# Kernel optimization log

Hardware: AMD Instinct MI355X
Metric: run time of the kernel (lower is better)

The kernel has to match this reference:

```python
import jax, jax.numpy as jnp
import numpy as np

EPS = 1e-5

@jax.custom_vjp
def binarize(x):
    # sign quantization: {-1, +1} (0 -> +1), as in BinaryNet Binarize
    return jnp.where(x >= 0, 1.0, -1.0).astype(x.dtype)

def _bin_fwd(x):
    return binarize(x), x

def _bin_bwd(res, g):
    # straight-through estimator with hardtanh clipping
    return (g * (jnp.abs(res) <= 1.0).astype(g.dtype),)

binarize.defvjp(_bin_fwd, _bin_bwd)


def batchnorm(x, gamma, beta):
    # BatchNorm1d, training mode: biased batch statistics over the batch axis
    mu = jnp.mean(x, axis=0)
    var = jnp.var(x, axis=0)
    return (x - mu) * jax.lax.rsqrt(var + EPS) * gamma + beta


def setup_inputs() -> dict:
    key = jax.random.key(0)
    ks = jax.random.split(key, 5)
    B, IND, HID, OUT = 16384, 768, 4096, 10
    return {
        "x": jax.random.normal(ks[0], (B, 784), jnp.float32),
        "w1": jax.random.normal(ks[1], (HID, IND), jnp.float32) * 0.05,
        "w2": jax.random.normal(ks[2], (HID, HID), jnp.float32) * 0.05,
        "w3": jax.random.normal(ks[3], (HID, HID), jnp.float32) * 0.05,
        "w4": jax.random.normal(ks[4], (OUT, HID), jnp.float32) * 0.05,
        "g1": jnp.ones(HID, jnp.float32), "b1": jnp.zeros(HID, jnp.float32),
        "g2": jnp.ones(HID, jnp.float32), "b2": jnp.zeros(HID, jnp.float32),
        "g3": jnp.ones(HID, jnp.float32), "b3": jnp.zeros(HID, jnp.float32),
        "g4": jnp.ones(OUT, jnp.float32), "b4": jnp.zeros(OUT, jnp.float32),
    }


def reference(x, w1, w2, w3, w4, g1, b1, g2, b2, g3, b3, g4, b4):
    # x.view(-1, 784); if width == 784, keep first 768 features
    h = x.reshape(-1, 784)[:, :768]
    # BinarizeLinear: binarize activations (width != 784) and weights, then matmul
    h = binarize(h) @ binarize(w1).T            # [B, 4096]
    h = jnp.clip(batchnorm(h, g1, b1), -1.0, 1.0)  # bn1 + hardtanh1
    h = binarize(h) @ binarize(w2).T
    h = jnp.clip(batchnorm(h, g2, b2), -1.0, 1.0)
    h = binarize(h) @ binarize(w3).T
    h = jnp.clip(batchnorm(h, g3, b3), -1.0, 1.0)
    h = binarize(h) @ binarize(w4).T            # [B, 10]
    h = batchnorm(h, g4, b4)
    return jax.nn.log_softmax(h, axis=1)
```

## Files before the change

kernel.cpp:

```cpp
#include <hip/hip_runtime.h>
#include <hip/hip_bf16.h>
#include <stdint.h>

typedef int v4i __attribute__((ext_vector_type(4)));

#define DEVI static __device__ __forceinline__

DEVI void gload16(const void* g, void* l) {
    __builtin_amdgcn_global_load_lds(
        (const __attribute__((address_space(1))) void*)g,
        (__attribute__((address_space(3))) void*)l,
        16, 0, 0);
}

#define WAITV(n) asm volatile("s_waitcnt vmcnt(" #n ")" ::: "memory")
#define WAITL0() asm volatile("s_waitcnt lgkmcnt(0)" ::: "memory")
#define SBAR()   __builtin_amdgcn_s_barrier()
#define SCHEDB() __builtin_amdgcn_sched_barrier(0)

__global__ __launch_bounds__(256) void k_bin_f32_to_i8(
    const float* __restrict__ w, int8_t* __restrict__ o, int n16)
{
    int t = blockIdx.x * 256 + threadIdx.x;
    if (t >= n16) return;
    const float4* s = (const float4*)w + (size_t)t * 4;
    union { int4 v; int8_t b[16]; } u;
#pragma unroll
    for (int i = 0; i < 4; ++i) {
        float4 f = s[i];
        u.b[i*4+0] = (f.x >= 0.f) ? (int8_t)1 : (int8_t)-1;
        u.b[i*4+1] = (f.y >= 0.f) ? (int8_t)1 : (int8_t)-1;
        u.b[i*4+2] = (f.z >= 0.f) ? (int8_t)1 : (int8_t)-1;
        u.b[i*4+3] = (f.w >= 0.f) ? (int8_t)1 : (int8_t)-1;
    }
    *(int4*)(o + (size_t)t * 16) = u.v;
}

__global__ __launch_bounds__(256) void k_bin_x(
    const float* __restrict__ x, int8_t* __restrict__ o)
{
    int t = blockIdx.x * 256 + threadIdx.x;
    int row = t / 48;
    int ch  = t % 48;
    const float4* s = (const float4*)(x + (size_t)row * 784 + ch * 16);
    union { int4 v; int8_t b[16]; } u;
#pragma unroll
    for (int i = 0; i < 4; ++i) {
        float4 f = s[i];
        u.b[i*4+0] = (f.x >= 0.f) ? (int8_t)1 : (int8_t)-1;
        u.b[i*4+1] = (f.y >= 0.f) ? (int8_t)1 : (int8_t)-1;
        u.b[i*4+2] = (f.z >= 0.f) ? (int8_t)1 : (int8_t)-1;
        u.b[i*4+3] = (f.w >= 0.f) ? (int8_t)1 : (int8_t)-1;
    }
    *(int4*)(o + (size_t)row * 768 + ch * 16) = u.v;
}

__global__ __launch_bounds__(512, 2)
void k_gemm256(const int8_t* __restrict__ A, const int8_t* __restrict__ B,
               int16_t* __restrict__ C, int* __restrict__ gsum,
               unsigned long long* __restrict__ gsq,
               int N, int K, int nbx)
{
    __shared__ __align__(16) int8_t lds[131072];

    const int tid  = threadIdx.x;
    const int lane = tid & 63;
    const int wave = tid >> 6;

    const int cpx = gridDim.x >> 3;
    const int id  = blockIdx.x;
    const int sw  = (id & 7) * cpx + (id >> 3);
    const int bx  = sw % nbx;
    const int by  = sw / nbx;

    const int NT = K >> 6;

    const int sr  = tid >> 2;
    const int asw = (((tid & 3) ^ (sr & 3)) << 4);
    const int8_t* gA0 = A + (size_t)(by * 256 + sr)       * K + asw;
    const int8_t* gA1 = A + (size_t)(by * 256 + 128 + sr) * K + asw;
    const int8_t* gB0 = B + (size_t)(bx * 256 + sr)       * K + asw;
    const int8_t* gB1 = B + (size_t)(bx * 256 + 128 + sr) * K + asw;
    const int ld0 = (wave * 64) << 4;
    const int ld1 = (512 + wave * 64) << 4;

    const int lrow = lane & 15;
    const int ksl  = lane >> 4;
    const int wr = (wave >> 2) * 128;
    const int wc = (wave & 3) * 64;
    const int fsw = ((ksl ^ (lrow & 3)) << 4);
    int aoff[8], boff[4];
#pragma unroll
    for (int m = 0; m < 8; ++m) aoff[m] = ((wr + m * 16 + lrow) << 6) + fsw;
#pragma unroll
    for (int n = 0; n < 4; ++n) boff[n] = ((wc + n * 16 + lrow) << 6) + fsw;

    v4i acc[8][4];
    v4i zero = {0, 0, 0, 0};
#pragma unroll
    for (int m = 0; m < 8; ++m)
#pragma unroll
        for (int n = 0; n < 4; ++n) acc[m][n] = zero;

#define STAGE_A(kt, b) do { const int _o = (kt) << 6;                    \
        int8_t* _d = lds + (b) * 16384;                                  \
        gload16(gA0 + _o, _d + ld0); gload16(gA1 + _o, _d + ld1); } while (0)
#define STAGE_B(kt, b) do { const int _o = (kt) << 6;                    \
        int8_t* _d = lds + 65536 + (b) * 16384;                          \
        gload16(gB0 + _o, _d + ld0); gload16(gB1 + _o, _d + ld1); } while (0)

    STAGE_A(0, 0); STAGE_B(0, 0);
    STAGE_A(1, 1); STAGE_B(1, 1);
    STAGE_A(2, 2); STAGE_B(2, 2);
    WAITV(8);
    SBAR();

    for (int kt = 0; kt < NT; ++kt) {
        const int b = kt & 3;
        const int8_t* ab = lds + b * 16384;
        const int8_t* bb = lds + 65536 + b * 16384;
        const int sb = (kt + 3) & 3;
        const bool st = (kt + 3 < NT);

        v4i af[4], bf[4];
#pragma unroll
        for (int m = 0; m < 4; ++m) af[m] = *(const v4i*)(ab + aoff[m]);
#pragma unroll
        for (int n = 0; n < 4; ++n) bf[n] = *(const v4i*)(bb + boff[n]);
        if (st) STAGE_A(kt + 3, sb);
        SBAR();
        WAITL0();
        SCHEDB();
        __builtin_amdgcn_s_setprio(1);
#pragma unroll
        for (int m = 0; m < 4; ++m)
#pragma unroll
            for (int n = 0; n < 4; ++n)
                acc[m][n] = __builtin_amdgcn_mfma_i32_16x16x64_i8(
                    af[m], bf[n], acc[m][n], 0, 0, 0);
        __builtin_amdgcn_s_setprio(0);
        SBAR();

        v4i ag[4];
#pragma unroll
        for (int m = 0; m < 4; ++m) ag[m] = *(const v4i*)(ab + aoff[4 + m]);
        if (st) STAGE_B(kt + 3, sb);
        if (kt < NT - 3)       { WAITV(8); }
        else if (kt == NT - 3) { WAITV(4); }
        else if (kt == NT - 2) { WAITV(0); }
        SBAR();
        WAITL0();
        SCHEDB();
        __builtin_amdgcn_s_setprio(1);
#pragma unroll
        for (int m = 0; m < 4; ++m)
#pragma unroll
            for (int n = 0; n < 4; ++n)
                acc[4 + m][n] = __builtin_amdgcn_mfma_i32_16x16x64_i8(
                    ag[m], bf[n], acc[4 + m][n], 0, 0, 0);
        __builtin_amdgcn_s_setprio(0);
        SBAR();
    }
#undef STAGE_A
#undef STAGE_B

    const int row0 = by * 256 + wr + ksl * 4;
    const int col0 = bx * 256 + wc + lrow;
#pragma unroll
    for (int m = 0; m < 8; ++m)
#pragma unroll
        for (int rr = 0; rr < 4; ++rr) {
            int16_t* dst = C + (size_t)(row0 + m * 16 + rr) * N + col0;
#pragma unroll
            for (int n = 0; n < 4; ++n)
                dst[n * 16] = (int16_t)acc[m][n][rr];
        }
#pragma unroll
    for (int n = 0; n < 4; ++n) {
        int s = 0; unsigned q = 0;
#pragma unroll
        for (int m = 0; m < 8; ++m)
#pragma unroll
            for (int rr = 0; rr < 4; ++rr) {
                int v = acc[m][n][rr];
                s += v;
                q += (unsigned)(v * v);
            }
        s += __shfl_xor(s, 16);
        s += __shfl_xor(s, 32);
        q += (unsigned)__shfl_xor((int)q, 16);
        q += (unsigned)__shfl_xor((int)q, 32);
        if (ksl == 0) {
            const int col = col0 + n * 16;
            atomicAdd(&gsum[col], s);
            atomicAdd(&gsq[col], (unsigned long long)q);
        }
    }
}

__global__ __launch_bounds__(256)
void k_gemm4(const int8_t* __restrict__ A, const int8_t* __restrict__ Bw,
             int* __restrict__ C4, int K)
{
    const int lane = threadIdx.x & 63;
    const int wave = threadIdx.x >> 6;
    const int lrow = lane & 15, ksl = lane >> 4;
    const int r0 = blockIdx.x * 128 + wave * 32;
    const int k0 = blockIdx.y * 512;

    const int8_t* ap0 = A + (size_t)(r0 + lrow) * K + k0 + ksl * 16;
    const int8_t* ap1 = ap0 + (size_t)16 * K;
    const int8_t* bp  = Bw + (size_t)lrow * K + k0 + ksl * 16;

    v4i acc0 = {0,0,0,0}, acc1 = {0,0,0,0};
#pragma unroll
    for (int kk = 0; kk < 8; ++kk) {
        v4i a0 = *(const v4i*)(ap0 + kk * 64);
        v4i a1 = *(const v4i*)(ap1 + kk * 64);
        v4i b  = *(const v4i*)(bp  + kk * 64);
        acc0 = __builtin_amdgcn_mfma_i32_16x16x64_i8(a0, b, acc0, 0, 0, 0);
        acc1 = __builtin_amdgcn_mfma_i32_16x16x64_i8(a1, b, acc1, 0, 0, 0);
    }
#pragma unroll
    for (int rr = 0; rr < 4; ++rr) {
        atomicAdd(&C4[(size_t)(r0 + ksl * 4 + rr) * 16 + lrow], acc0[rr]);
        atomicAdd(&C4[(size_t)(r0 + 16 + ksl * 4 + rr) * 16 + lrow], acc1[rr]);
    }
}

__global__ __launch_bounds__(256)
void k_colstats4(const int* __restrict__ C4, int rows,
                 int* __restrict__ gsum, unsigned long long* __restrict__ gsq)
{
    const int col = threadIdx.x & 15, grp = threadIdx.x >> 4;
    const int rpb = rows / gridDim.x;
    const int r0  = blockIdx.x * rpb;
    int s = 0; unsigned long long q = 0;
    for (int r = grp; r < rpb; r += 16) {
        int v = C4[(size_t)(r0 + r) * 16 + col];
        s += v;
        q += (unsigned long long)((long long)v * (long long)v);
    }
    __shared__ int ss[256];
    __shared__ unsigned long long sq[256];
    ss[threadIdx.x] = s; sq[threadIdx.x] = q;
    __syncthreads();
    if (grp == 0) {
#pragma unroll
        for (int t = 1; t < 16; ++t) { s += ss[t * 16 + col]; q += sq[t * 16 + col]; }
        atomicAdd(&gsum[col], s);
        atomicAdd(&gsq[col], q);
    }
}

__global__ __launch_bounds__(128)
void k_finalize(const int* __restrict__ gsum, const unsigned long long* __restrict__ gsq,
                const float* __restrict__ gamma, const float* __restrict__ beta,
                float* __restrict__ pa, float* __restrict__ pb,
                int rows, int ncols_act, int ncols_pad)
{
    int c = blockIdx.x * 128 + threadIdx.x;
    if (c >= ncols_pad) return;
    double mu  = (double)gsum[c] / (double)rows;
    double var = (double)(long long)gsq[c] / (double)rows - mu * mu;
    float rs = rsqrtf((float)var + 1e-5f);
    float g  = (c < ncols_act) ? gamma[c] : 0.f;
    float be = (c < ncols_act) ? beta[c]  : 0.f;
    pa[c] = rs * g;
    pb[c] = be - (float)mu * rs * g;
}

__global__ __launch_bounds__(256)
void k_bnbin(const int16_t* __restrict__ C, const float* __restrict__ pa,
             const float* __restrict__ pb, int8_t* __restrict__ Aout,
             int n16, int colmask)
{
    int t = blockIdx.x * 256 + threadIdx.x;
    if (t >= n16) return;
    const size_t base = (size_t)t * 16;
    const int c0 = (int)(base & (size_t)colmask);
    union { int4 v; short s[8]; } u0, u1;
    u0.v = *(const int4*)(C + base);
    u1.v = *(const int4*)(C + base + 8);
    float4 a[4], b[4];
#pragma unroll
    for (int i = 0; i < 4; ++i) {
        a[i] = *(const float4*)(pa + c0 + i * 4);
        b[i] = *(const float4*)(pb + c0 + i * 4);
    }
    union { int4 v; int8_t b[16]; } o;
#pragma unroll
    for (int i = 0; i < 16; ++i) {
        float y = (float)((i < 8) ? u0.s[i] : u1.s[i - 8]);
        float aa = ((const float*)&a[i >> 2])[i & 3];
        float bb = ((const float*)&b[i >> 2])[i & 3];
        o.b[i] = (y * aa + bb >= 0.f) ? (int8_t)1 : (int8_t)-1;
    }
    *(int4*)(Aout + base) = o.v;
}

__global__ __launch_bounds__(256)
void k_logsoftmax(const int* __restrict__ C4, const float* __restrict__ pa,
                  const float* __restrict__ pb, float* __restrict__ out, int rows)
{
    int r = blockIdx.x * 256 + threadIdx.x;
    if (r >= rows) return;
    const int* row = C4 + (size_t)r * 16;
    float v[10];
    float m = -1e30f;
#pragma unroll
    for (int c = 0; c < 10; ++c) {
        v[c] = (float)row[c] * pa[c] + pb[c];
        m = fmaxf(m, v[c]);
    }
    float s = 0.f;
#pragma unroll
    for (int c = 0; c < 10; ++c) s += expf(v[c] - m);
    float ls = logf(s);
#pragma unroll
    for (int c = 0; c < 10; ++c) out[(size_t)r * 10 + c] = v[c] - m - ls;
}

extern "C" void kernel_launch(void* const* d_in, const int* in_sizes, int n_in,
                              void* d_out, int out_size, void* d_ws, size_t ws_size,
                              hipStream_t stream)
{
    (void)in_sizes; (void)n_in; (void)out_size; (void)ws_size;
    const float* x  = (const float*)d_in[0];
    const float* w1 = (const float*)d_in[1];
    const float* w2 = (const float*)d_in[2];
    const float* w3 = (const float*)d_in[3];
    const float* w4 = (const float*)d_in[4];
    const float* g1 = (const float*)d_in[5];
    const float* b1 = (const float*)d_in[6];
    const float* g2 = (const float*)d_in[7];
    const float* b2 = (const float*)d_in[8];
    const float* g3 = (const float*)d_in[9];
    const float* b3 = (const float*)d_in[10];
    const float* g4 = (const float*)d_in[11];
    const float* b4 = (const float*)d_in[12];
    float* out = (float*)d_out;

    const int B = 16384, HID = 4096, IND = 768;

    char* p = (char*)d_ws;
    size_t off = 0;
    auto alloc = [&](size_t sz) -> char* {
        char* r = p + off;
        off += (sz + 255) & ~(size_t)255;
        return r;
    };
    int8_t*  W1   = (int8_t*)alloc((size_t)HID * IND);
    int8_t*  W2   = (int8_t*)alloc((size_t)HID * HID);
    int8_t*  W3   = (int8_t*)alloc((size_t)HID * HID);
    int8_t*  W4p  = (int8_t*)alloc((size_t)16 * HID);
    int8_t*  Abuf = (int8_t*)alloc((size_t)B * HID);
    int16_t* C    = (int16_t*)alloc((size_t)B * HID * 2);
    int*     C4   = (int*)alloc((size_t)B * 16 * 4);
    int*     gsum = (int*)alloc((size_t)HID * 4);
    unsigned long long* gsq = (unsigned long long*)alloc((size_t)HID * 8);
    float*   pa   = (float*)alloc((size_t)HID * 4);
    float*   pb   = (float*)alloc((size_t)HID * 4);

    hipMemsetAsync(W4p, 0, (size_t)16 * HID, stream);
    k_bin_f32_to_i8<<<(HID * IND / 16 + 255) / 256, 256, 0, stream>>>(w1, W1, HID * IND / 16);
    k_bin_f32_to_i8<<<(HID * HID / 16 + 255) / 256, 256, 0, stream>>>(w2, W2, HID * HID / 16);
    k_bin_f32_to_i8<<<(HID * HID / 16 + 255) / 256, 256, 0, stream>>>(w3, W3, HID * HID / 16);
    k_bin_f32_to_i8<<<(10 * HID / 16 + 255) / 256, 256, 0, stream>>>(w4, W4p, 10 * HID / 16);
    k_bin_x<<<B * 48 / 256, 256, 0, stream>>>(x, Abuf);

    const int nbx = HID / 256, nby = B / 256;

    hipMemsetAsync(gsum, 0, HID * 12, stream);
    k_gemm256<<<nbx * nby, 512, 0, stream>>>(Abuf, W1, C, gsum, gsq, HID, IND, nbx);
    k_finalize<<<HID / 128, 128, 0, stream>>>(gsum, gsq, g1, b1, pa, pb, B, HID, HID);
    k_bnbin<<<B * HID / 16 / 256, 256, 0, stream>>>(C, pa, pb, Abuf, B * HID / 16, HID - 1);

    hipMemsetAsync(gsum, 0, HID * 12, stream);
    k_gemm256<<<nbx * nby, 512, 0, stream>>>(Abuf, W2, C, gsum, gsq, HID, HID, nbx);
    k_finalize<<<HID / 128, 128, 0, stream>>>(gsum, gsq, g2, b2, pa, pb, B, HID, HID);
    k_bnbin<<<B * HID / 16 / 256, 256, 0, stream>>>(C, pa, pb, Abuf, B * HID / 16, HID - 1);

    hipMemsetAsync(gsum, 0, HID * 12, stream);
    k_gemm256<<<nbx * nby, 512, 0, stream>>>(Abuf, W3, C, gsum, gsq, HID, HID, nbx);
    k_finalize<<<HID / 128, 128, 0, stream>>>(gsum, gsq, g3, b3, pa, pb, B, HID, HID);
    k_bnbin<<<B * HID / 16 / 256, 256, 0, stream>>>(C, pa, pb, Abuf, B * HID / 16, HID - 1);

    hipMemsetAsync(C4, 0, (size_t)B * 16 * 4, stream);
    k_gemm4<<<dim3(B / 128, 8), 256, 0, stream>>>(Abuf, W4p, C4, HID);
    hipMemsetAsync(gsum, 0, HID * 12, stream);
    k_colstats4<<<16, 256, 0, stream>>>(C4, B, gsum, gsq);
    k_finalize<<<1, 128, 0, stream>>>(gsum, gsq, g4, b4, pa, pb, B, 10, 16);
    k_logsoftmax<<<B / 256, 256, 0, stream>>>(C4, pa, pb, out, B);
}
```

Measured before the change: 835.3 us.

## Shrink int8 GEMM tile to 256x128 with 3-stage pipeline for higher occupancy

Changes the int8 MFMA GEMM block tile from 256x256 to 256x128, with each of 8 waves now owning a 64x64 output sub-tile. The LDS pipeline goes from 4 to 3 stages, cutting shared memory from 128KB to 72KB, and the launch bound is raised to 4 blocks per CU. The per-iteration sync is simplified by dropping the split half-step loads, lgkmcnt waits and sched barriers, and the swizzle pattern changes. The aim is more concurrent blocks to hide latency, at the cost of less data reuse per tile, more global loads, and possible LDS hazards from the removed waits.

```diff
diff --git a/kernel.cpp b/kernel.cpp
--- a/kernel.cpp
+++ b/kernel.cpp
@@ -14,9 +14,7 @@
 }
 
 #define WAITV(n) asm volatile("s_waitcnt vmcnt(" #n ")" ::: "memory")
-#define WAITL0() asm volatile("s_waitcnt lgkmcnt(0)" ::: "memory")
 #define SBAR()   __builtin_amdgcn_s_barrier()
-#define SCHEDB() __builtin_amdgcn_sched_barrier(0)
 
 __global__ __launch_bounds__(256) void k_bin_f32_to_i8(
     const float* __restrict__ w, int8_t* __restrict__ o, int n16)
@@ -55,13 +53,13 @@
     *(int4*)(o + (size_t)row * 768 + ch * 16) = u.v;
 }
 
-__global__ __launch_bounds__(512, 2)
+__global__ __launch_bounds__(512, 4)
 void k_gemm256(const int8_t* __restrict__ A, const int8_t* __restrict__ B,
                int16_t* __restrict__ C, int* __restrict__ gsum,
                unsigned long long* __restrict__ gsq,
                int N, int K, int nbx)
 {
-    __shared__ __align__(16) int8_t lds[131072];
+    __shared__ __align__(16) int8_t lds[73728];
 
     const int tid  = threadIdx.x;
     const int lane = tid & 63;
@@ -76,61 +74,57 @@
     const int NT = K >> 6;
 
     const int sr  = tid >> 2;
-    const int asw = (((tid & 3) ^ (sr & 3)) << 4);
+    const int asw = (((tid & 3) ^ ((sr >> 1) & 3)) << 4);
     const int8_t* gA0 = A + (size_t)(by * 256 + sr)       * K + asw;
     const int8_t* gA1 = A + (size_t)(by * 256 + 128 + sr) * K + asw;
-    const int8_t* gB0 = B + (size_t)(bx * 256 + sr)       * K + asw;
-    const int8_t* gB1 = B + (size_t)(bx * 256 + 128 + sr) * K + asw;
-    const int ld0 = (wave * 64) << 4;
-    const int ld1 = (512 + wave * 64) << 4;
+    const int8_t* gB0 = B + (size_t)(bx * 128 + sr)       * K + asw;
+    const int ldw = wave << 10;
 
     const int lrow = lane & 15;
     const int ksl  = lane >> 4;
-    const int wr = (wave >> 2) * 128;
-    const int wc = (wave & 3) * 64;
-    const int fsw = ((ksl ^ (lrow & 3)) << 4);
-    int aoff[8], boff[4];
-#pragma unroll
-    for (int m = 0; m < 8; ++m) aoff[m] = ((wr + m * 16 + lrow) << 6) + fsw;
+    const int wr = (wave >> 1) * 64;
+    const int wc = (wave & 1) * 64;
+    const int fsw = ((ksl ^ ((lrow >> 1) & 3)) << 4);
+    int aoff[4], boff[4];
+#pragma unroll
+    for (int m = 0; m < 4; ++m) aoff[m] = ((wr + m * 16 + lrow) << 6) + fsw;
 #pragma unroll
     for (int n = 0; n < 4; ++n) boff[n] = ((wc + n * 16 + lrow) << 6) + fsw;
 
-    v4i acc[8][4];
+    v4i acc[4][4];
     v4i zero = {0, 0, 0, 0};
 #pragma unroll
-    for (int m = 0; m < 8; ++m)
+    for (int m = 0; m < 4; ++m)
 #pragma unroll
         for (int n = 0; n < 4; ++n) acc[m][n] = zero;
 
-#define STAGE_A(kt, b) do { const int _o = (kt) << 6;                    \
-        int8_t* _d = lds + (b) * 16384;                                  \
-        gload16(gA0 + _o, _d + ld0); gload16(gA1 + _o, _d + ld1); } while (0)
-#define STAGE_B(kt, b) do { const int _o = (kt) << 6;                    \
-        int8_t* _d = lds + 65536 + (b) * 16384;                          \
-        gload16(gB0 + _o, _d + ld0); gload16(gB1 + _o, _d + ld1); } while (0)
-
-    STAGE_A(0, 0); STAGE_B(0, 0);
-    STAGE_A(1, 1); STAGE_B(1, 1);
-    STAGE_A(2, 2); STAGE_B(2, 2);
-    WAITV(8);
+#define STAGE(kt, b) do { const int _o = (kt) << 6;                         \
+        int8_t* _dA = lds + (b) * 16384;                                    \
+        gload16(gA0 + _o, _dA + ldw);                                       \
+        gload16(gA1 + _o, _dA + 8192 + ldw);                                \
+        gload16(gB0 + _o, lds + 49152 + (b) * 8192 + ldw); } while (0)
+
+    STAGE(0, 0); STAGE(1, 1);
+    WAITV(3);
     SBAR();
 
+    int cb = 0;
     for (int kt = 0; kt < NT; ++kt) {
-        const int b = kt & 3;
-        const int8_t* ab = lds + b * 16384;
-        const int8_t* bb = lds + 65536 + b * 16384;
-        const int sb = (kt + 3) & 3;
-        const bool st = (kt + 3 < NT);
-
+        if (kt + 2 < NT) {
+            int sb = cb + 2; if (sb >= 3) sb -= 3;
+            STAGE(kt + 2, sb);
+        }
+        if (kt < NT - 2)       { WAITV(3); }
+        else if (kt == NT - 2) { WAITV(0); }
+
+        const int8_t* ab = lds + cb * 16384;
+        const int8_t* bb = lds + 49152 + cb * 8192;
         v4i af[4], bf[4];
 #pragma unroll
         for (int m = 0; m < 4; ++m) af[m] = *(const v4i*)(ab + aoff[m]);
 #pragma unroll
         for (int n = 0; n < 4; ++n) bf[n] = *(const v4i*)(bb + boff[n]);
-        if (st) STAGE_A(kt + 3, sb);
-        SBAR();
-        WAITL0();
-        SCHEDB();
+
         __builtin_amdgcn_s_setprio(1);
 #pragma unroll
         for (int m = 0; m < 4; ++m)
@@ -140,34 +134,14 @@
                     af[m], bf[n], acc[m][n], 0, 0, 0);
         __builtin_amdgcn_s_setprio(0);
         SBAR();
-
-        v4i ag[4];
-#pragma unroll
-        for (int m = 0; m < 4; ++m) ag[m] = *(const v4i*)(ab + aoff[4 + m]);
-        if (st) STAGE_B(kt + 3, sb);
-        if (kt < NT - 3)       { WAITV(8); }
-        else if (kt == NT - 3) { WAITV(4); }
-        else if (kt == NT - 2) { WAITV(0); }
-        SBAR();
-        WAITL0();
-        SCHEDB();
-        __builtin_amdgcn_s_setprio(1);
-#pragma unroll
-        for (int m = 0; m < 4; ++m)
-#pragma unroll
-            for (int n = 0; n < 4; ++n)
-                acc[4 + m][n] = __builtin_amdgcn_mfma_i32_16x16x64_i8(
-                    ag[m], bf[n], acc[4 + m][n], 0, 0, 0);
-        __builtin_amdgcn_s_setprio(0);
-        SBAR();
-    }
-#undef STAGE_A
-#undef STAGE_B
+        ++cb; if (cb >= 3) cb = 0;
+    }
+#undef STAGE
 
     const int row0 = by * 256 + wr + ksl * 4;
-    const int col0 = bx * 256 + wc + lrow;
-#pragma unroll
-    for (int m = 0; m < 8; ++m)
+    const int col0 = bx * 128 + wc + lrow;
+#pragma unroll
+    for (int m = 0; m < 4; ++m)
 #pragma unroll
         for (int rr = 0; rr < 4; ++rr) {
             int16_t* dst = C + (size_t)(row0 + m * 16 + rr) * N + col0;
@@ -179,7 +153,7 @@
     for (int n = 0; n < 4; ++n) {
         int s = 0; unsigned q = 0;
 #pragma unroll
-        for (int m = 0; m < 8; ++m)
+        for (int m = 0; m < 4; ++m)
 #pragma unroll
             for (int rr = 0; rr < 4; ++rr) {
                 int v = acc[m][n][rr];
@@ -369,7 +343,7 @@
     k_bin_f32_to_i8<<<(10 * HID / 16 + 255) / 256, 256, 0, stream>>>(w4, W4p, 10 * HID / 16);
     k_bin_x<<<B * 48 / 256, 256, 0, stream>>>(x, Abuf);
 
-    const int nbx = HID / 256, nby = B / 256;
+    const int nbx = HID / 128, nby = B / 256;
 
     hipMemsetAsync(gsum, 0, HID * 12, stream);
     k_gemm256<<<nbx * nby, 512, 0, stream>>>(Abuf, W1, C, gsum, gsq, HID, IND, nbx);
```

Result: slower. 852.1 us (+2.0%).
